# Performance work log

Hardware: AMD Instinct MI355X
Metric: run time of the kernel (lower is better)

Reference implementation:

```python
import jax, jax.numpy as jnp
import numpy as np

IN_F = 4096
OUT_F = 4096
GS = 128              # group_size
GC = IN_F // GS       # group_count = 32
PACK = 8              # int4 values per int32


def setup_inputs() -> dict:
    key = jax.random.key(0)
    k1, k2, k3, k4, k5 = jax.random.split(key, 5)
    x = jax.random.normal(k1, (4, 2048, IN_F), dtype=jnp.float32)
    # packed int4 weights: (out_features, in_features // 8), nibbles in low->high bits
    qweight = jax.random.randint(k2, (OUT_F, IN_F // PACK), -(2**31), 2**31 - 1, dtype=jnp.int32)
    scales = jax.random.uniform(k3, (GC, OUT_F), dtype=jnp.float32) * 0.01
    qzeros = jax.random.randint(k4, (GC, OUT_F), 0, 16, dtype=jnp.int32)
    bias = jax.random.normal(k5, (OUT_F,), dtype=jnp.float32) * 0.01
    return {"x": x, "qweight": qweight, "scales": scales, "qzeros": qzeros, "bias": bias}


def _dequantize(qweight, scales, qzeros):
    # unpack 8 nibbles per int32 along last dim (shifts 0,4,...,28), as in _unpack_int4_last_dim
    shifts = jnp.arange(0, 32, 4, dtype=jnp.int32)  # [8]
    w_int = ((qweight[:, :, None] >> shifts) & 15)  # (OUT, IN//8, 8)
    w_int = w_int.reshape(OUT_F, IN_F).astype(jnp.float32)  # (OUT, IN)
    gid = jnp.arange(IN_F) // GS  # (IN,) group id per input channel
    z = qzeros.astype(jnp.float32)[gid].T   # (OUT, IN)
    s = scales[gid].T                        # (OUT, IN)
    return (w_int - z) * s                   # (OUT, IN)


def reference(x, qweight, scales, qzeros, bias):
    W = _dequantize(qweight, scales, qzeros)          # (OUT, IN)
    # F.linear: y = x @ W^T + b
    return jnp.einsum('bsi,oi->bso', x, W) + bias
```

## Files before the change

kernel.cpp:

```cpp
#include <hip/hip_runtime.h>
#include <hip/hip_bf16.h>
#include <stdint.h>

#define IN_F 4096
#define OUT_F 4096
#define M_TOTAL 8192
#define NKT 64

typedef __hip_bfloat16 bf16;
typedef __attribute__((ext_vector_type(8))) short bf16x8;
typedef __attribute__((ext_vector_type(4))) float f32x4;

__global__ __launch_bounds__(256) void prep(const int* __restrict__ qweight,
                                            const float* __restrict__ scales,
                                            const int* __restrict__ qzeros,
                                            bf16* __restrict__ Wb,
                                            const float* __restrict__ x,
                                            bf16* __restrict__ Xb) {
    int b = blockIdx.x;
    if (b < 8192) {
        int idx = b * 256 + threadIdx.x;
        int o = idx >> 9;
        int j = idx & 511;
        int g = j >> 4;
        int qw = qweight[idx];
        float s = scales[g * OUT_F + o];
        float z = (float)qzeros[g * OUT_F + o];
        union { bf16 h[8]; uint4 q; } out;
#pragma unroll
        for (int k = 0; k < 8; ++k) {
            float w = (float)((qw >> (4 * k)) & 15);
            out.h[k] = __float2bfloat16((w - z) * s);
        }
        *reinterpret_cast<uint4*>(Wb + ((size_t)o * IN_F + j * 8)) = out.q;
    } else {
        int idx = (b - 8192) * 256 + threadIdx.x;
        const float4* p = reinterpret_cast<const float4*>(x) + (size_t)idx * 2;
        float4 a = p[0], c = p[1];
        union { bf16 h[8]; uint4 q; } o;
        o.h[0] = __float2bfloat16(a.x); o.h[1] = __float2bfloat16(a.y);
        o.h[2] = __float2bfloat16(a.z); o.h[3] = __float2bfloat16(a.w);
        o.h[4] = __float2bfloat16(c.x); o.h[5] = __float2bfloat16(c.y);
        o.h[6] = __float2bfloat16(c.z); o.h[7] = __float2bfloat16(c.w);
        reinterpret_cast<uint4*>(Xb)[idx] = o.q;
    }
}


__device__ __forceinline__ void gload16(const bf16* g, char* l) {
    __builtin_amdgcn_global_load_lds(
        (const __attribute__((address_space(1))) void*)g,
        (__attribute__((address_space(3))) void*)l, 16, 0, 0);
}

__device__ __forceinline__ void stage_half(const bf16* __restrict__ Gt,
                                           char* ldsb, int wave, int lane) {
    const int slog8 = ((lane & 7) ^ (lane >> 3)) * 8;
#pragma unroll
    for (int j = 0; j < 2; ++j) {
        int r = wave * 16 + j * 8 + (lane >> 3);
        gload16(Gt + (size_t)r * IN_F + slog8, ldsb + (wave * 2 + j) * 1024);
    }
}

#define BARRIER() do { asm volatile("" ::: "memory"); \
                       __builtin_amdgcn_s_barrier();  \
                       asm volatile("" ::: "memory"); } while (0)
#define LGKM0()   asm volatile("s_waitcnt lgkmcnt(0)" ::: "memory")
#define VMCNT6()  asm volatile("s_waitcnt vmcnt(6)" ::: "memory")
#define VMCNT0()  asm volatile("s_waitcnt vmcnt(0)" ::: "memory")

#define LDA_SET(DST, BUF, MH) do {                                              \
  _Pragma("unroll") for (int m4 = 0; m4 < 4; ++m4)                              \
  _Pragma("unroll") for (int kk = 0; kk < 2; ++kk)                              \
    DST[m4][kk] = *reinterpret_cast<const bf16x8*>(sm + (BUF) * 65536           \
        + (((MH) * 128 + wr * 64 + m4 * 16 + l15) << 7)                         \
        + ((((kk << 2) + lq) ^ l7) << 4));                                      \
} while (0)

#define LDB_SET(DST, BUF, NH) do {                                              \
  _Pragma("unroll") for (int n2 = 0; n2 < 2; ++n2)                              \
  _Pragma("unroll") for (int kk = 0; kk < 2; ++kk)                              \
    DST[n2][kk] = *reinterpret_cast<const bf16x8*>(sm + (BUF) * 65536 + 32768   \
        + (((NH) * 128 + wc * 32 + n2 * 16 + l15) << 7)                         \
        + ((((kk << 2) + lq) ^ l7) << 4));                                      \
} while (0)

#define MMA_Q(AF, BFR, MH, NH) do {                                             \
  __builtin_amdgcn_s_setprio(1);                                                \
  _Pragma("unroll") for (int m4 = 0; m4 < 4; ++m4)                              \
  _Pragma("unroll") for (int n2 = 0; n2 < 2; ++n2)                              \
  _Pragma("unroll") for (int kk = 0; kk < 2; ++kk)                              \
    acc[(MH) * 4 + m4][(NH) * 2 + n2] = __builtin_amdgcn_mfma_f32_16x16x32_bf16(\
        AF[m4][kk], BFR[n2][kk], acc[(MH) * 4 + m4][(NH) * 2 + n2], 0, 0, 0);   \
  __builtin_amdgcn_s_setprio(0);                                                \
} while (0)

__global__ __launch_bounds__(512, 2) void gemm256(const bf16* __restrict__ A,
                                                  const bf16* __restrict__ B,
                                                  const float* __restrict__ bias,
                                                  float* __restrict__ C) {
    extern __shared__ char sm[];
    const int tid  = threadIdx.x;
    const int wave = tid >> 6;
    const int lane = tid & 63;
    const int wr   = wave >> 2;
    const int wc   = wave & 3;
    const int l15  = lane & 15;
    const int lq   = lane >> 4;
    const int l7   = lane & 7;

    const int nwg = gridDim.x;
    const int cpx = nwg >> 3;
    const int wg  = blockIdx.x;
    const int swz = (wg & 7) * cpx + (wg >> 3);
    const int bm  = swz >> 4;
    const int bn  = swz & 15;
    const int m0  = bm * 256;
    const int n0  = bn * 256;

    const bf16* A0 = A + (size_t)m0 * IN_F;
    const bf16* A1 = A + (size_t)(m0 + 128) * IN_F;
    const bf16* B0 = B + (size_t)n0 * IN_F;
    const bf16* B1 = B + (size_t)(n0 + 128) * IN_F;

    f32x4 acc[8][4];
#pragma unroll
    for (int m = 0; m < 8; ++m)
#pragma unroll
        for (int n = 0; n < 4; ++n) acc[m][n] = (f32x4){0.f, 0.f, 0.f, 0.f};

    bf16x8 af0[4][2], af1[4][2], bfr0[2][2], bfr1[2][2];

    stage_half(A0,      sm + 0,     wave, lane);
    stage_half(A1,      sm + 16384, wave, lane);
    stage_half(B0,      sm + 32768, wave, lane);
    stage_half(B1,      sm + 49152, wave, lane);
    stage_half(A0 + 64, sm + 65536, wave, lane);
    stage_half(A1 + 64, sm + 81920, wave, lane);
    stage_half(B0 + 64, sm + 98304, wave, lane);
    VMCNT6();
    BARRIER();
    LDA_SET(af0, 0, 0);
    LDB_SET(bfr0, 0, 0);

    for (int i = 0; i < 32; ++i) {
        const int t1 = 2 * i + 1;
        const int t2 = 2 * i + 2;
        const int t3 = 2 * i + 3;
        const bool gg = (i < 31);

        stage_half(B1 + t1 * 64, sm + 114688, wave, lane);
        BARRIER(); LGKM0();
        MMA_Q(af0, bfr0, 0, 0);
        LDA_SET(af1, 0, 1);
        BARRIER();
        if (gg) stage_half(A0 + t2 * 64, sm + 0, wave, lane);
        BARRIER(); LGKM0();
        MMA_Q(af1, bfr0, 1, 0);
        LDB_SET(bfr1, 0, 1);
        BARRIER();
        if (gg) stage_half(A1 + t2 * 64, sm + 16384, wave, lane);
        BARRIER(); LGKM0();
        MMA_Q(af0, bfr1, 0, 1);
        BARRIER();
        if (gg) stage_half(B0 + t2 * 64, sm + 32768, wave, lane);
        BARRIER(); LGKM0();
        MMA_Q(af1, bfr1, 1, 1);
        if (gg) { VMCNT6(); } else { VMCNT0(); }
        LDA_SET(af0, 1, 0);
        LDB_SET(bfr0, 1, 0);
        BARRIER();

        if (gg) stage_half(B1 + t2 * 64, sm + 49152, wave, lane);
        BARRIER(); LGKM0();
        MMA_Q(af0, bfr0, 0, 0);
        LDA_SET(af1, 1, 1);
        BARRIER();
        if (gg) stage_half(A0 + t3 * 64, sm + 65536, wave, lane);
        BARRIER(); LGKM0();
        MMA_Q(af1, bfr0, 1, 0);
        LDB_SET(bfr1, 1, 1);
        BARRIER();
        if (gg) stage_half(A1 + t3 * 64, sm + 81920, wave, lane);
        BARRIER(); LGKM0();
        MMA_Q(af0, bfr1, 0, 1);
        BARRIER();
        if (gg) stage_half(B0 + t3 * 64, sm + 98304, wave, lane);
        BARRIER(); LGKM0();
        MMA_Q(af1, bfr1, 1, 1);
        if (gg) { VMCNT6(); } else { VMCNT0(); }
        if (gg) {
            LDA_SET(af0, 0, 0);
            LDB_SET(bfr0, 0, 0);
        }
        BARRIER();
    }

    const int crow_base = m0 + wr * 64 + lq * 4;
    const int ccol_base = n0 + wc * 32 + l15;
#pragma unroll
    for (int n = 0; n < 4; ++n) {
        const int NH = n >> 1, n2 = n & 1;
        const int col = ccol_base + NH * 128 + n2 * 16;
        float bv = bias[col];
#pragma unroll
        for (int m = 0; m < 8; ++m) {
            const int MH = m >> 2, m4 = m & 3;
            const int row = crow_base + MH * 128 + m4 * 16;
#pragma unroll
            for (int r = 0; r < 4; ++r)
                C[(size_t)(row + r) * OUT_F + col] = acc[m][n][r] + bv;
        }
    }
}

__global__ __launch_bounds__(256) void fallback_gemm(const float* __restrict__ x,
                                                     const int* __restrict__ qweight,
                                                     const float* __restrict__ scales,
                                                     const int* __restrict__ qzeros,
                                                     const float* __restrict__ bias,
                                                     float* __restrict__ out) {
    __shared__ float Asf[64][65];
    __shared__ float Bsf[64][65];
    int bm = blockIdx.x >> 6;
    int bn = blockIdx.x & 63;
    int m0 = bm * 64, n0 = bn * 64;
    int t  = threadIdx.x;
    int tr = t >> 4, tc = t & 15;
    float acc[4][4] = {};
    for (int kt = 0; kt < IN_F; kt += 64) {
#pragma unroll
        for (int i = 0; i < 4; ++i) {
            int idx = t + i * 256;
            int r = idx >> 4, c4 = idx & 15;
            float4 v = *reinterpret_cast<const float4*>(x + (size_t)(m0 + r) * IN_F + kt + c4 * 4);
            Asf[r][c4 * 4 + 0] = v.x; Asf[r][c4 * 4 + 1] = v.y;
            Asf[r][c4 * 4 + 2] = v.z; Asf[r][c4 * 4 + 3] = v.w;
        }
#pragma unroll
        for (int i = 0; i < 2; ++i) {
            int idx = t + i * 256;
            int r = idx >> 3, k8 = idx & 7;
            int kk = kt + k8 * 8;
            int o  = n0 + r;
            int qw = qweight[(size_t)o * (IN_F / 8) + (kk >> 3)];
            int g  = kk >> 7;
            float s = scales[g * OUT_F + o];
            float z = (float)qzeros[g * OUT_F + o];
#pragma unroll
            for (int b = 0; b < 8; ++b)
                Bsf[r][k8 * 8 + b] = ((float)((qw >> (4 * b)) & 15) - z) * s;
        }
        __syncthreads();
#pragma unroll 8
        for (int k = 0; k < 64; ++k) {
            float a[4], bb[4];
#pragma unroll
            for (int i = 0; i < 4; ++i) a[i] = Asf[tr * 4 + i][k];
#pragma unroll
            for (int j = 0; j < 4; ++j) bb[j] = Bsf[tc * 4 + j][k];
#pragma unroll
            for (int i = 0; i < 4; ++i)
#pragma unroll
                for (int j = 0; j < 4; ++j) acc[i][j] += a[i] * bb[j];
        }
        __syncthreads();
    }
#pragma unroll
    for (int i = 0; i < 4; ++i) {
        int row = m0 + tr * 4 + i;
#pragma unroll
        for (int j = 0; j < 4; ++j) {
            int col = n0 + tc * 4 + j;
            out[(size_t)row * OUT_F + col] = acc[i][j] + bias[col];
        }
    }
}

extern "C" void kernel_launch(void* const* d_in, const int* in_sizes, int n_in,
                              void* d_out, int out_size, void* d_ws, size_t ws_size,
                              hipStream_t stream) {
    (void)in_sizes; (void)n_in; (void)out_size;
    const float* x       = (const float*)d_in[0];
    const int*   qweight = (const int*)d_in[1];
    const float* scales  = (const float*)d_in[2];
    const int*   qzeros  = (const int*)d_in[3];
    const float* bias    = (const float*)d_in[4];
    float* out = (float*)d_out;

    const size_t needW = (size_t)OUT_F * IN_F * sizeof(bf16);
    const size_t needX = (size_t)M_TOTAL * IN_F * sizeof(bf16);

    if (ws_size >= needW + needX) {
        bf16* Wb = (bf16*)d_ws;
        bf16* Xb = (bf16*)((char*)d_ws + needW);
        prep<<<8192 + 16384, 256, 0, stream>>>(qweight, scales, qzeros, Wb, x, Xb);
        gemm256<<<(M_TOTAL / 256) * (OUT_F / 256), 512, 131072, stream>>>(Xb, Wb, bias, out);
    } else {
        fallback_gemm<<<(M_TOTAL / 64) * (OUT_F / 64), 256, 0, stream>>>(
            x, qweight, scales, qzeros, bias, out);
    }
}
```

Measured before the change: 273.0 us.

## Fuse fp32-to-bf16 conversion of activations into GEMM A-tile staging

Removes the separate x-to-bf16 conversion pass (and its 64MB bf16 workspace write and re-read) by loading fp32 activations directly in the GEMM through registers, converting to bf16, and writing to LDS. The B tile keeps the direct global-to-LDS path. This trades a standalone memory pass for double the global read bytes per A tile (each A tile is re-read by 16 column blocks in fp32) plus extra register pressure and VALU conversion work inside the main loop, and the vmcnt-based waits are restructured accordingly.

```diff
diff --git a/kernel.cpp b/kernel.cpp
--- a/kernel.cpp
+++ b/kernel.cpp
@@ -11,39 +11,24 @@
 typedef __attribute__((ext_vector_type(8))) short bf16x8;
 typedef __attribute__((ext_vector_type(4))) float f32x4;
 
-__global__ __launch_bounds__(256) void prep(const int* __restrict__ qweight,
-                                            const float* __restrict__ scales,
-                                            const int* __restrict__ qzeros,
-                                            bf16* __restrict__ Wb,
-                                            const float* __restrict__ x,
-                                            bf16* __restrict__ Xb) {
-    int b = blockIdx.x;
-    if (b < 8192) {
-        int idx = b * 256 + threadIdx.x;
-        int o = idx >> 9;
-        int j = idx & 511;
-        int g = j >> 4;
-        int qw = qweight[idx];
-        float s = scales[g * OUT_F + o];
-        float z = (float)qzeros[g * OUT_F + o];
-        union { bf16 h[8]; uint4 q; } out;
-#pragma unroll
-        for (int k = 0; k < 8; ++k) {
-            float w = (float)((qw >> (4 * k)) & 15);
-            out.h[k] = __float2bfloat16((w - z) * s);
-        }
-        *reinterpret_cast<uint4*>(Wb + ((size_t)o * IN_F + j * 8)) = out.q;
-    } else {
-        int idx = (b - 8192) * 256 + threadIdx.x;
-        const float4* p = reinterpret_cast<const float4*>(x) + (size_t)idx * 2;
-        float4 a = p[0], c = p[1];
-        union { bf16 h[8]; uint4 q; } o;
-        o.h[0] = __float2bfloat16(a.x); o.h[1] = __float2bfloat16(a.y);
-        o.h[2] = __float2bfloat16(a.z); o.h[3] = __float2bfloat16(a.w);
-        o.h[4] = __float2bfloat16(c.x); o.h[5] = __float2bfloat16(c.y);
-        o.h[6] = __float2bfloat16(c.z); o.h[7] = __float2bfloat16(c.w);
-        reinterpret_cast<uint4*>(Xb)[idx] = o.q;
-    }
+__global__ __launch_bounds__(256) void dequant_w(const int* __restrict__ qweight,
+                                                 const float* __restrict__ scales,
+                                                 const int* __restrict__ qzeros,
+                                                 bf16* __restrict__ Wb) {
+    int idx = blockIdx.x * 256 + threadIdx.x;
+    int o = idx >> 9;
+    int j = idx & 511;
+    int g = j >> 4;
+    int qw = qweight[idx];
+    float s = scales[g * OUT_F + o];
+    float z = (float)qzeros[g * OUT_F + o];
+    union { bf16 h[8]; uint4 q; } out;
+#pragma unroll
+    for (int b = 0; b < 8; ++b) {
+        float w = (float)((qw >> (4 * b)) & 15);
+        out.h[b] = __float2bfloat16((w - z) * s);
+    }
+    *reinterpret_cast<uint4*>(Wb + ((size_t)o * IN_F + j * 8)) = out.q;
 }
 
 
@@ -63,11 +48,34 @@
     }
 }
 
+__device__ __forceinline__ void issueA(const float* __restrict__ Xg,
+                                       int wave, int lane, float4 av[2][2]) {
+    const int slog8 = ((lane & 7) ^ (lane >> 3)) * 8;
+#pragma unroll
+    for (int jj = 0; jj < 2; ++jj) {
+        const float* p = Xg + (size_t)(wave * 16 + jj * 8 + (lane >> 3)) * IN_F + slog8;
+        av[jj][0] = *reinterpret_cast<const float4*>(p);
+        av[jj][1] = *reinterpret_cast<const float4*>(p + 4);
+    }
+}
+
+__device__ __forceinline__ void writeA(char* ldsb, int wave, int lane,
+                                       const float4 av[2][2]) {
+#pragma unroll
+    for (int jj = 0; jj < 2; ++jj) {
+        union { bf16 h[8]; uint4 q; } u;
+        u.h[0] = __float2bfloat16(av[jj][0].x); u.h[1] = __float2bfloat16(av[jj][0].y);
+        u.h[2] = __float2bfloat16(av[jj][0].z); u.h[3] = __float2bfloat16(av[jj][0].w);
+        u.h[4] = __float2bfloat16(av[jj][1].x); u.h[5] = __float2bfloat16(av[jj][1].y);
+        u.h[6] = __float2bfloat16(av[jj][1].z); u.h[7] = __float2bfloat16(av[jj][1].w);
+        *reinterpret_cast<uint4*>(ldsb + (wave * 2 + jj) * 1024 + lane * 16) = u.q;
+    }
+}
+
 #define BARRIER() do { asm volatile("" ::: "memory"); \
                        __builtin_amdgcn_s_barrier();  \
                        asm volatile("" ::: "memory"); } while (0)
 #define LGKM0()   asm volatile("s_waitcnt lgkmcnt(0)" ::: "memory")
-#define VMCNT6()  asm volatile("s_waitcnt vmcnt(6)" ::: "memory")
 #define VMCNT0()  asm volatile("s_waitcnt vmcnt(0)" ::: "memory")
 
 #define LDA_SET(DST, BUF, MH) do {                                              \
@@ -96,7 +104,7 @@
   __builtin_amdgcn_s_setprio(0);                                                \
 } while (0)
 
-__global__ __launch_bounds__(512, 2) void gemm256(const bf16* __restrict__ A,
+__global__ __launch_bounds__(512, 2) void gemm256(const float* __restrict__ X,
                                                   const bf16* __restrict__ B,
                                                   const float* __restrict__ bias,
                                                   float* __restrict__ C) {
@@ -119,10 +127,10 @@
     const int m0  = bm * 256;
     const int n0  = bn * 256;
 
-    const bf16* A0 = A + (size_t)m0 * IN_F;
-    const bf16* A1 = A + (size_t)(m0 + 128) * IN_F;
-    const bf16* B0 = B + (size_t)n0 * IN_F;
-    const bf16* B1 = B + (size_t)(n0 + 128) * IN_F;
+    const float* X0 = X + (size_t)m0 * IN_F;
+    const float* X1 = X + (size_t)(m0 + 128) * IN_F;
+    const bf16*  B0 = B + (size_t)n0 * IN_F;
+    const bf16*  B1 = B + (size_t)(n0 + 128) * IN_F;
 
     f32x4 acc[8][4];
 #pragma unroll
@@ -131,15 +139,20 @@
         for (int n = 0; n < 4; ++n) acc[m][n] = (f32x4){0.f, 0.f, 0.f, 0.f};
 
     bf16x8 af0[4][2], af1[4][2], bfr0[2][2], bfr1[2][2];
-
-    stage_half(A0,      sm + 0,     wave, lane);
-    stage_half(A1,      sm + 16384, wave, lane);
+    float4 avH0[2][2], avH1[2][2];
+
+    issueA(X0, wave, lane, avH0);
+    issueA(X1, wave, lane, avH1);
     stage_half(B0,      sm + 32768, wave, lane);
     stage_half(B1,      sm + 49152, wave, lane);
-    stage_half(A0 + 64, sm + 65536, wave, lane);
-    stage_half(A1 + 64, sm + 81920, wave, lane);
     stage_half(B0 + 64, sm + 98304, wave, lane);
-    VMCNT6();
+    writeA(sm + 0,     wave, lane, avH0);
+    writeA(sm + 16384, wave, lane, avH1);
+    issueA(X0 + 64, wave, lane, avH0);
+    issueA(X1 + 64, wave, lane, avH1);
+    writeA(sm + 65536, wave, lane, avH0);
+    writeA(sm + 81920, wave, lane, avH1);
+    LGKM0();
     BARRIER();
     LDA_SET(af0, 0, 0);
     LDB_SET(bfr0, 0, 0);
@@ -150,46 +163,49 @@
         const int t3 = 2 * i + 3;
         const bool gg = (i < 31);
 
+        if (gg) issueA(X0 + t2 * 64, wave, lane, avH0);
         stage_half(B1 + t1 * 64, sm + 114688, wave, lane);
         BARRIER(); LGKM0();
         MMA_Q(af0, bfr0, 0, 0);
         LDA_SET(af1, 0, 1);
         BARRIER();
-        if (gg) stage_half(A0 + t2 * 64, sm + 0, wave, lane);
+        if (gg) issueA(X1 + t2 * 64, wave, lane, avH1);
         BARRIER(); LGKM0();
         MMA_Q(af1, bfr0, 1, 0);
+        if (gg) writeA(sm + 0, wave, lane, avH0);
         LDB_SET(bfr1, 0, 1);
         BARRIER();
-        if (gg) stage_half(A1 + t2 * 64, sm + 16384, wave, lane);
+        if (gg) stage_half(B0 + t2 * 64, sm + 32768, wave, lane);
         BARRIER(); LGKM0();
         MMA_Q(af0, bfr1, 0, 1);
-        BARRIER();
-        if (gg) stage_half(B0 + t2 * 64, sm + 32768, wave, lane);
+        if (gg) writeA(sm + 16384, wave, lane, avH1);
+        BARRIER();
         BARRIER(); LGKM0();
         MMA_Q(af1, bfr1, 1, 1);
-        if (gg) { VMCNT6(); } else { VMCNT0(); }
+        if (!gg) VMCNT0();
         LDA_SET(af0, 1, 0);
         LDB_SET(bfr0, 1, 0);
         BARRIER();
 
+        if (gg) issueA(X0 + t3 * 64, wave, lane, avH0);
         if (gg) stage_half(B1 + t2 * 64, sm + 49152, wave, lane);
         BARRIER(); LGKM0();
         MMA_Q(af0, bfr0, 0, 0);
         LDA_SET(af1, 1, 1);
         BARRIER();
-        if (gg) stage_half(A0 + t3 * 64, sm + 65536, wave, lane);
+        if (gg) issueA(X1 + t3 * 64, wave, lane, avH1);
         BARRIER(); LGKM0();
         MMA_Q(af1, bfr0, 1, 0);
+        if (gg) writeA(sm + 65536, wave, lane, avH0);
         LDB_SET(bfr1, 1, 1);
         BARRIER();
-        if (gg) stage_half(A1 + t3 * 64, sm + 81920, wave, lane);
+        if (gg) stage_half(B0 + t3 * 64, sm + 98304, wave, lane);
         BARRIER(); LGKM0();
         MMA_Q(af0, bfr1, 0, 1);
-        BARRIER();
-        if (gg) stage_half(B0 + t3 * 64, sm + 98304, wave, lane);
+        if (gg) writeA(sm + 81920, wave, lane, avH1);
+        BARRIER();
         BARRIER(); LGKM0();
         MMA_Q(af1, bfr1, 1, 1);
-        if (gg) { VMCNT6(); } else { VMCNT0(); }
         if (gg) {
             LDA_SET(af0, 0, 0);
             LDB_SET(bfr0, 0, 0);
@@ -290,13 +306,11 @@
     float* out = (float*)d_out;
 
     const size_t needW = (size_t)OUT_F * IN_F * sizeof(bf16);
-    const size_t needX = (size_t)M_TOTAL * IN_F * sizeof(bf16);
-
-    if (ws_size >= needW + needX) {
+
+    if (ws_size >= needW) {
         bf16* Wb = (bf16*)d_ws;
-        bf16* Xb = (bf16*)((char*)d_ws + needW);
-        prep<<<8192 + 16384, 256, 0, stream>>>(qweight, scales, qzeros, Wb, x, Xb);
-        gemm256<<<(M_TOTAL / 256) * (OUT_F / 256), 512, 131072, stream>>>(Xb, Wb, bias, out);
+        dequant_w<<<(OUT_F * (IN_F / 8)) / 256, 256, 0, stream>>>(qweight, scales, qzeros, Wb);
+        gemm256<<<(M_TOTAL / 256) * (OUT_F / 256), 512, 131072, stream>>>(x, Wb, bias, out);
     } else {
         fallback_gemm<<<(M_TOTAL / 64) * (OUT_F / 64), 256, 0, stream>>>(
             x, qweight, scales, qzeros, bias, out);
```

Measured after the change: 598.3 us. 2.19x slower.
